# Performance work log

Hardware: AMD Instinct MI355X
Metric: run time of the kernel (lower is better)

## Reference

```python
import jax, jax.numpy as jnp
import numpy as np

N_NODES = 50000
D = 128
N_EDGES = 600000


def setup_inputs() -> dict:
    key = jax.random.key(0)
    k1, k2, k3, k4 = jax.random.split(key, 4)
    x = jax.random.normal(k1, (N_NODES, D), dtype=jnp.float32)
    edge_index = jax.random.randint(k2, (2, N_EDGES), 0, N_NODES, dtype=jnp.int64)
    # edge MLP params: Linear(2D -> D) -> ReLU -> Linear(D -> D)
    W1 = jax.random.normal(k3, (2 * D, D), dtype=jnp.float32) * (1.0 / np.sqrt(2 * D))
    b1 = jnp.zeros((D,), dtype=jnp.float32)
    W2 = jax.random.normal(k4, (D, D), dtype=jnp.float32) * (1.0 / np.sqrt(D))
    b2 = jnp.zeros((D,), dtype=jnp.float32)
    return {"x": x, "edge_index": edge_index, "W1": W1, "b1": b1, "W2": W2, "b2": b2}


def reference(x, edge_index, W1, b1, W2, b2):
    # gather sender / receiver node features and concat along feature dim
    src = x[edge_index[0]]            # [E, D]
    dst = x[edge_index[1]]            # [E, D]
    edge_inputs = jnp.concatenate([src, dst], axis=1)  # [E, 2D]
    # edge MLP (model_fn)
    h = jax.nn.relu(edge_inputs @ W1 + b1)             # [E, D]
    edge_attr = h @ W2 + b2                            # [E, D]
    return edge_attr
```

## Files before the change

kernel.cpp:

```cpp
#include <hip/hip_runtime.h>

typedef __attribute__((ext_vector_type(8))) short  short8;
typedef __attribute__((ext_vector_type(4))) float  float4v;
typedef __attribute__((ext_vector_type(2))) int    int2v;

#define E_TILE 64
#define LDA    264
#define LDH    136
#define PGRID  512

__device__ __forceinline__ short f2bf(float f) {
    union { float f; unsigned u; } v; v.f = f;
    unsigned r = (v.u + 0x7FFFu + ((v.u >> 16) & 1u)) >> 16;
    return (short)r;
}

__global__ __launch_bounds__(256, 2)
void edge_mlp_kernel(const float* __restrict__ x,
                     const int*   __restrict__ ei,
                     const float* __restrict__ W1,
                     const float* __restrict__ b1,
                     const float* __restrict__ W2,
                     const float* __restrict__ b2,
                     float*       __restrict__ out,
                     int E, int nTiles) {
    __shared__ short sA[E_TILE * LDA];
    __shared__ short sH[E_TILE * LDH];
    __shared__ int   sIdx[2][2 * E_TILE];

    const int tid  = threadIdx.x;
    const int wave = tid >> 6;
    const int lane = tid & 63;
    const int quad = lane >> 4;
    const int l16  = lane & 15;
    const int nBase = wave * 32;
    const int G = gridDim.x;

    short8 bw1[8][2];
    short8 bw2[4][2];
    #pragma unroll
    for (int kt = 0; kt < 8; ++kt)
        #pragma unroll
        for (int nt = 0; nt < 2; ++nt) {
            short8 f;
            #pragma unroll
            for (int j = 0; j < 8; ++j) {
                int k = kt * 32 + quad * 8 + j;
                int n = nBase + nt * 16 + l16;
                f[j] = f2bf(W1[k * 128 + n]);
            }
            bw1[kt][nt] = f;
        }
    #pragma unroll
    for (int kt = 0; kt < 4; ++kt)
        #pragma unroll
        for (int nt = 0; nt < 2; ++nt) {
            short8 f;
            #pragma unroll
            for (int j = 0; j < 8; ++j) {
                int k = kt * 32 + quad * 8 + j;
                int n = nBase + nt * 16 + l16;
                f[j] = f2bf(W2[k * 128 + n]);
            }
            bw2[kt][nt] = f;
        }
    float b1v[2], b2v[2];
    #pragma unroll
    for (int nt = 0; nt < 2; ++nt) {
        b1v[nt] = b1[nBase + nt * 16 + l16];
        b2v[nt] = b2[nBase + nt * 16 + l16];
    }

    auto stageIdx = [&](int b, int t) {
        if (tid < E_TILE) {
            int s = 0, d = 0;
            if (t < nTiles) {
                long eg = (long)t * E_TILE + tid;
                if (eg < (long)E) { s = ei[eg]; d = ei[(long)E + eg]; }
            }
            sIdx[b][tid] = s;
            sIdx[b][E_TILE + tid] = d;
        }
    };

    auto gather = [&](int b) {
        #pragma unroll
        for (int i = 0; i < 16; ++i) {
            int f = tid + 256 * i;
            int e = f >> 6;
            int c = f & 63;
            int node = (c < 32) ? sIdx[b][e] : sIdx[b][E_TILE + e];
            int cc = c & 31;
            float4v v = *(const float4v*)&x[(long)node * 128 + cc * 4];
            unsigned lo, hi;
            asm("v_cvt_pk_bf16_f32 %0, %1, %2" : "=v"(lo) : "v"(v.x), "v"(v.y));
            asm("v_cvt_pk_bf16_f32 %0, %1, %2" : "=v"(hi) : "v"(v.z), "v"(v.w));
            int2v s; s.x = (int)lo; s.y = (int)hi;
            *(int2v*)&sA[e * LDA + c * 4] = s;
        }
    };

    const int t0 = blockIdx.x;
    if (t0 >= nTiles) return;
    stageIdx(0, t0);
    __syncthreads();
    gather(0);
    stageIdx(1, t0 + G);
    __syncthreads();

    int buf = 1;
    for (int t = t0; t < nTiles; t += G) {
        const long eBase = (long)t * E_TILE;

        float4v acc[4][2];
        #pragma unroll
        for (int mt = 0; mt < 4; ++mt)
            #pragma unroll
            for (int nt = 0; nt < 2; ++nt)
                acc[mt][nt] = (float4v)(0.0f);

        #pragma unroll
        for (int kt = 0; kt < 8; ++kt) {
            short8 a[4];
            #pragma unroll
            for (int mt = 0; mt < 4; ++mt)
                a[mt] = *(const short8*)&sA[(mt * 16 + l16) * LDA + kt * 32 + quad * 8];
            #pragma unroll
            for (int mt = 0; mt < 4; ++mt)
                #pragma unroll
                for (int nt = 0; nt < 2; ++nt)
                    acc[mt][nt] = __builtin_amdgcn_mfma_f32_16x16x32_bf16(
                        a[mt], bw1[kt][nt], acc[mt][nt], 0, 0, 0);
        }

        #pragma unroll
        for (int mt = 0; mt < 4; ++mt)
            #pragma unroll
            for (int nt = 0; nt < 2; ++nt)
                #pragma unroll
                for (int r = 0; r < 4; ++r) {
                    int m = mt * 16 + quad * 4 + r;
                    int n = nBase + nt * 16 + l16;
                    float h = acc[mt][nt][r] + b1v[nt];
                    h = fmaxf(h, 0.0f);
                    sH[m * LDH + n] = f2bf(h);
                }

        __syncthreads();

        const bool hasNext = (t + G < nTiles);
        if (hasNext) gather(buf);
        stageIdx(buf ^ 1, t + 2 * G);

        float4v acc2[4][2];
        #pragma unroll
        for (int mt = 0; mt < 4; ++mt)
            #pragma unroll
            for (int nt = 0; nt < 2; ++nt)
                acc2[mt][nt] = (float4v)(0.0f);

        #pragma unroll
        for (int kt = 0; kt < 4; ++kt) {
            short8 a[4];
            #pragma unroll
            for (int mt = 0; mt < 4; ++mt)
                a[mt] = *(const short8*)&sH[(mt * 16 + l16) * LDH + kt * 32 + quad * 8];
            #pragma unroll
            for (int mt = 0; mt < 4; ++mt)
                #pragma unroll
                for (int nt = 0; nt < 2; ++nt)
                    acc2[mt][nt] = __builtin_amdgcn_mfma_f32_16x16x32_bf16(
                        a[mt], bw2[kt][nt], acc2[mt][nt], 0, 0, 0);
        }

        #pragma unroll
        for (int mt = 0; mt < 4; ++mt)
            #pragma unroll
            for (int nt = 0; nt < 2; ++nt)
                #pragma unroll
                for (int r = 0; r < 4; ++r) {
                    int m = mt * 16 + quad * 4 + r;
                    long e = eBase + m;
                    if (e < (long)E) {
                        int n = nBase + nt * 16 + l16;
                        __builtin_nontemporal_store(acc2[mt][nt][r] + b2v[nt],
                                                    &out[e * 128 + n]);
                    }
                }

        __syncthreads();
        buf ^= 1;
    }
}

extern "C" void kernel_launch(void* const* d_in, const int* in_sizes, int n_in,
                              void* d_out, int out_size, void* d_ws, size_t ws_size,
                              hipStream_t stream) {
    const float* x  = (const float*)d_in[0];
    const int*   ei = (const int*)d_in[1];
    const float* W1 = (const float*)d_in[2];
    const float* b1 = (const float*)d_in[3];
    const float* W2 = (const float*)d_in[4];
    const float* b2 = (const float*)d_in[5];
    float* out = (float*)d_out;
    int E = in_sizes[1] / 2;
    int nTiles = (E + E_TILE - 1) / E_TILE;
    int grid = nTiles < PGRID ? nTiles : PGRID;
    edge_mlp_kernel<<<grid, 256, 0, stream>>>(x, ei, W1, b1, W2, b2, out, E, nTiles);
}
```

Before: 435.2 us.

## Pre-convert x to bf16 and gather via direct global-to-LDS loads

Adds a pre-pass kernel that converts x to bf16 in workspace once, so each edge gather reads half the bytes. The gather then uses global_load_lds with an XOR-swizzled LDS layout instead of register loads plus conversion, and the A-fragment reads apply the matching swizzle. Output stores are staged through LDS so each thread writes 16-byte vectors. Occupancy is raised to 3 blocks per CU with a 768-block grid, and barriers become lgkmcnt waits. The trade-offs are an extra kernel launch plus a full pass over x, and an additional barrier per tile.

```diff
diff --git a/kernel.cpp b/kernel.cpp
--- a/kernel.cpp
+++ b/kernel.cpp
@@ -2,12 +2,13 @@
 
 typedef __attribute__((ext_vector_type(8))) short  short8;
 typedef __attribute__((ext_vector_type(4))) float  float4v;
-typedef __attribute__((ext_vector_type(2))) int    int2v;
+typedef __attribute__((ext_vector_type(4))) int    int4v;
 
 #define E_TILE 64
-#define LDA    264
 #define LDH    136
-#define PGRID  512
+#define PGRID  768
+
+#define BAR_LGKM asm volatile("s_waitcnt lgkmcnt(0)\n\ts_barrier" ::: "memory")
 
 __device__ __forceinline__ short f2bf(float f) {
     union { float f; unsigned u; } v; v.f = f;
@@ -15,8 +16,23 @@
     return (short)r;
 }
 
-__global__ __launch_bounds__(256, 2)
-void edge_mlp_kernel(const float* __restrict__ x,
+__global__ __launch_bounds__(256)
+void cvt_x_kernel(const float* __restrict__ x, short* __restrict__ x16, long n8) {
+    long i = (long)blockIdx.x * 256 + threadIdx.x;
+    if (i >= n8) return;
+    const float4v* p = (const float4v*)(x + i * 8);
+    float4v a = p[0], b = p[1];
+    unsigned r0, r1, r2, r3;
+    asm("v_cvt_pk_bf16_f32 %0, %1, %2" : "=v"(r0) : "v"(a.x), "v"(a.y));
+    asm("v_cvt_pk_bf16_f32 %0, %1, %2" : "=v"(r1) : "v"(a.z), "v"(a.w));
+    asm("v_cvt_pk_bf16_f32 %0, %1, %2" : "=v"(r2) : "v"(b.x), "v"(b.y));
+    asm("v_cvt_pk_bf16_f32 %0, %1, %2" : "=v"(r3) : "v"(b.z), "v"(b.w));
+    int4v o; o.x = (int)r0; o.y = (int)r1; o.z = (int)r2; o.w = (int)r3;
+    *(int4v*)(x16 + i * 8) = o;
+}
+
+__global__ __launch_bounds__(256, 3)
+void edge_mlp_kernel(const short* __restrict__ x16,
                      const int*   __restrict__ ei,
                      const float* __restrict__ W1,
                      const float* __restrict__ b1,
@@ -24,7 +40,7 @@
                      const float* __restrict__ b2,
                      float*       __restrict__ out,
                      int E, int nTiles) {
-    __shared__ short sA[E_TILE * LDA];
+    __shared__ short sA[E_TILE * 256];
     __shared__ short sH[E_TILE * LDH];
     __shared__ int   sIdx[2][2 * E_TILE];
 
@@ -44,11 +60,8 @@
         for (int nt = 0; nt < 2; ++nt) {
             short8 f;
             #pragma unroll
-            for (int j = 0; j < 8; ++j) {
-                int k = kt * 32 + quad * 8 + j;
-                int n = nBase + nt * 16 + l16;
-                f[j] = f2bf(W1[k * 128 + n]);
-            }
+            for (int j = 0; j < 8; ++j)
+                f[j] = f2bf(W1[(kt * 32 + quad * 8 + j) * 128 + nBase + nt * 16 + l16]);
             bw1[kt][nt] = f;
         }
     #pragma unroll
@@ -57,11 +70,8 @@
         for (int nt = 0; nt < 2; ++nt) {
             short8 f;
             #pragma unroll
-            for (int j = 0; j < 8; ++j) {
-                int k = kt * 32 + quad * 8 + j;
-                int n = nBase + nt * 16 + l16;
-                f[j] = f2bf(W2[k * 128 + n]);
-            }
+            for (int j = 0; j < 8; ++j)
+                f[j] = f2bf(W2[(kt * 32 + quad * 8 + j) * 128 + nBase + nt * 16 + l16]);
             bw2[kt][nt] = f;
         }
     float b1v[2], b2v[2];
@@ -85,18 +95,17 @@
 
     auto gather = [&](int b) {
         #pragma unroll
-        for (int i = 0; i < 16; ++i) {
-            int f = tid + 256 * i;
-            int e = f >> 6;
-            int c = f & 63;
-            int node = (c < 32) ? sIdx[b][e] : sIdx[b][E_TILE + e];
-            int cc = c & 31;
-            float4v v = *(const float4v*)&x[(long)node * 128 + cc * 4];
-            unsigned lo, hi;
-            asm("v_cvt_pk_bf16_f32 %0, %1, %2" : "=v"(lo) : "v"(v.x), "v"(v.y));
-            asm("v_cvt_pk_bf16_f32 %0, %1, %2" : "=v"(hi) : "v"(v.z), "v"(v.w));
-            int2v s; s.x = (int)lo; s.y = (int)hi;
-            *(int2v*)&sA[e * LDA + c * 4] = s;
+        for (int r = 0; r < 8; ++r) {
+            int lin = tid + 256 * r;
+            int row = lin >> 5;
+            int cl  = lin & 31;
+            int c   = cl ^ (row & 7);
+            int node = (c < 16) ? sIdx[b][row] : sIdx[b][E_TILE + row];
+            const short* gp = x16 + (long)node * 128 + (c & 15) * 8;
+            __builtin_amdgcn_global_load_lds(
+                (const __attribute__((address_space(1))) void*)gp,
+                (__attribute__((address_space(3))) void*)&sA[lin * 8],
+                16, 0, 0);
         }
     };
 
@@ -108,7 +117,7 @@
     stageIdx(1, t0 + G);
     __syncthreads();
 
-    int buf = 1;
+    int p = 1;
     for (int t = t0; t < nTiles; t += G) {
         const long eBase = (long)t * E_TILE;
 
@@ -123,8 +132,11 @@
         for (int kt = 0; kt < 8; ++kt) {
             short8 a[4];
             #pragma unroll
-            for (int mt = 0; mt < 4; ++mt)
-                a[mt] = *(const short8*)&sA[(mt * 16 + l16) * LDA + kt * 32 + quad * 8];
+            for (int mt = 0; mt < 4; ++mt) {
+                int row = mt * 16 + l16;
+                int cl  = (kt * 4 + quad) ^ (l16 & 7);
+                a[mt] = *(const short8*)&sA[row * 256 + cl * 8];
+            }
             #pragma unroll
             for (int mt = 0; mt < 4; ++mt)
                 #pragma unroll
@@ -141,16 +153,14 @@
                 for (int r = 0; r < 4; ++r) {
                     int m = mt * 16 + quad * 4 + r;
                     int n = nBase + nt * 16 + l16;
-                    float h = acc[mt][nt][r] + b1v[nt];
-                    h = fmaxf(h, 0.0f);
+                    float h = fmaxf(acc[mt][nt][r] + b1v[nt], 0.0f);
                     sH[m * LDH + n] = f2bf(h);
                 }
 
-        __syncthreads();
-
-        const bool hasNext = (t + G < nTiles);
-        if (hasNext) gather(buf);
-        stageIdx(buf ^ 1, t + 2 * G);
+        BAR_LGKM;
+
+        if (t + G < nTiles) gather(p);
+        stageIdx(p ^ 1, t + 2 * G);
 
         float4v acc2[4][2];
         #pragma unroll
@@ -173,23 +183,41 @@
                         a[mt], bw2[kt][nt], acc2[mt][nt], 0, 0, 0);
         }
 
-        #pragma unroll
-        for (int mt = 0; mt < 4; ++mt)
-            #pragma unroll
-            for (int nt = 0; nt < 2; ++nt)
-                #pragma unroll
-                for (int r = 0; r < 4; ++r) {
-                    int m = mt * 16 + quad * 4 + r;
-                    long e = eBase + m;
-                    if (e < (long)E) {
-                        int n = nBase + nt * 16 + l16;
-                        __builtin_nontemporal_store(acc2[mt][nt][r] + b2v[nt],
-                                                    &out[e * 128 + n]);
-                    }
+        BAR_LGKM;
+
+        {
+            float* sHf = (float*)sH;
+            const int slab = wave * 1088;
+            #pragma unroll
+            for (int ph = 0; ph < 2; ++ph) {
+                #pragma unroll
+                for (int mh = 0; mh < 2; ++mh) {
+                    int mt = 2 * ph + mh;
+                    #pragma unroll
+                    for (int nt = 0; nt < 2; ++nt)
+                        #pragma unroll
+                        for (int r = 0; r < 4; ++r) {
+                            int row = mh * 16 + quad * 4 + r;
+                            int c   = nt * 16 + l16;
+                            sHf[slab + row * 34 + c] = acc2[mt][nt][r] + b2v[nt];
+                        }
                 }
+                #pragma unroll
+                for (int i = 0; i < 4; ++i) {
+                    int f   = lane + 64 * i;
+                    int row = f >> 3;
+                    int c   = f & 7;
+                    float4v v = *(const float4v*)&sHf[slab + row * 34 + c * 4];
+                    long e = eBase + 32 * ph + row;
+                    if (e < (long)E)
+                        __builtin_nontemporal_store(
+                            v, (float4v*)&out[e * 128 + nBase + c * 4]);
+                }
+            }
+        }
 
         __syncthreads();
-        buf ^= 1;
+        p ^= 1;
     }
 }
 
@@ -203,8 +231,14 @@
     const float* W2 = (const float*)d_in[4];
     const float* b2 = (const float*)d_in[5];
     float* out = (float*)d_out;
+    short* x16 = (short*)d_ws;
+
+    long n8 = (long)in_sizes[0] / 8;
+    int cgrid = (int)((n8 + 255) / 256);
+    cvt_x_kernel<<<cgrid, 256, 0, stream>>>(x, x16, n8);
+
     int E = in_sizes[1] / 2;
     int nTiles = (E + E_TILE - 1) / E_TILE;
     int grid = nTiles < PGRID ? nTiles : PGRID;
-    edge_mlp_kernel<<<grid, 256, 0, stream>>>(x, ei, W1, b1, W2, b2, out, E, nTiles);
-}
+    edge_mlp_kernel<<<grid, 256, 0, stream>>>(x16, ei, W1, b1, W2, b2, out, E, nTiles);
+}
```

Result: slower. 473.8 us (+8.9%).
